# Kernel tuning notes

Hardware: AMD Instinct MI355X
Metric: run time of the kernel (lower is better)

## Reference

```python
import jax, jax.numpy as jnp
import numpy as np

N = 100000          # num nodes
E = 1250000         # num directed edges
F_IN = 64           # num_features
H = 64              # hidden_channels
C = 2               # num_classes


def gcn_layer(x, W, b, src, dst, num_nodes):
    """PyG-style GCNConv: add self-loops, symmetric norm, scatter-add aggregation."""
    loop = jnp.arange(num_nodes)
    src2 = jnp.concatenate([src, loop])   # [E+N]
    dst2 = jnp.concatenate([dst, loop])
    deg = jax.ops.segment_sum(jnp.ones_like(dst2, dtype=x.dtype), dst2,
                              num_segments=num_nodes)          # in-degree incl self-loop
    dinv = jax.lax.rsqrt(jnp.maximum(deg, 1.0))                # deg >= 1 due to self-loops
    norm = dinv[src2] * dinv[dst2]                             # [E+N]
    h = x @ W                                                  # [N, out]
    out = jax.ops.segment_sum(norm[:, None] * h[src2], dst2,
                              num_segments=num_nodes)          # [N, out]
    return out + b


def setup_inputs() -> dict:
    key = jax.random.key(0)
    ks = jax.random.split(key, 8)
    x = jax.random.normal(ks[0], (N, F_IN), dtype=jnp.float32)
    edge_index = jax.random.randint(ks[1], (2, E), 0, N, dtype=jnp.int64)
    batch = jnp.zeros((N,), dtype=jnp.int64)
    s1 = 1.0 / np.sqrt(F_IN)
    s2 = 1.0 / np.sqrt(H)
    W1 = jax.random.uniform(ks[2], (F_IN, H), jnp.float32, -s1, s1)
    b1 = jnp.zeros((H,), jnp.float32)
    W2 = jax.random.uniform(ks[3], (H, H), jnp.float32, -s2, s2)
    b2 = jnp.zeros((H,), jnp.float32)
    Wlin = jax.random.uniform(ks[4], (H, C), jnp.float32, -s2, s2)
    blin = jax.random.uniform(ks[5], (C,), jnp.float32, -s2, s2)
    return {"x": x, "edge_index": edge_index, "batch": batch,
            "W1": W1, "b1": b1, "W2": W2, "b2": b2,
            "Wlin": Wlin, "blin": blin}


def reference(x, edge_index, batch, W1, b1, W2, b2, Wlin, blin):
    src, dst = edge_index[0], edge_index[1]
    h = gcn_layer(x, W1, b1, src, dst, N)
    h = jax.nn.relu(h)
    h = gcn_layer(h, W2, b2, src, dst, N)
    # dropout p=0.5 is identity in eval mode
    return h @ Wlin + blin  # [N, C]
```

## Files before the change

kernel.cpp:

```cpp
#include <hip/hip_runtime.h>
#include <hip/hip_bf16.h>


#define FDIM 64
#define BKT_BITS 8
#define BKT 256
#define CAP 4096
#define CHUNK 2048

typedef short s16x8 __attribute__((ext_vector_type(8)));
typedef float f32x4 __attribute__((ext_vector_type(4)));

__device__ __forceinline__ unsigned short f2b(float f) {
    unsigned u = __float_as_uint(f);
    u += 0x7fff + ((u >> 16) & 1);
    return (unsigned short)(u >> 16);
}
__device__ __forceinline__ void unpk(unsigned u, float& lo, float& hi) {
    lo = __uint_as_float(u << 16);
    hi = __uint_as_float(u & 0xffff0000u);
}
__device__ __forceinline__ unsigned packb(float lo, float hi) {
    return (unsigned)f2b(lo) | ((unsigned)f2b(hi) << 16);
}
__device__ __forceinline__ unsigned relu2(unsigned u) {
    unsigned t = (u >> 15) & 0x00010001u;
    return u & ~(t * 0xFFFFu);
}

__global__ __launch_bounds__(256) void k_zero_g(int* __restrict__ g, int nb) {
    int i = blockIdx.x * blockDim.x + threadIdx.x;
    if (i < nb) g[i] = 0;
}

__global__ __launch_bounds__(256) void k_part(const int* __restrict__ src,
                                              const int* __restrict__ dst,
                                              int* __restrict__ gcnt,
                                              unsigned* __restrict__ rec,
                                              int nE, int nb) {
    __shared__ int lh[512];
    __shared__ int rc[512];
    int t = threadIdx.x;
    for (int b = t; b < nb; b += 256) lh[b] = 0;
    __syncthreads();
    int e0 = blockIdx.x * CHUNK;
    int e1 = min(nE, e0 + CHUNK);
    int myb[8];
    unsigned myr[8];
#pragma unroll
    for (int j = 0; j < 8; ++j) {
        int i = e0 + t + j * 256;
        if (i < e1) {
            int d = dst[i];
            int s = src[i];
            int b = d >> BKT_BITS;
            myb[j] = b;
            myr[j] = (unsigned)s | ((unsigned)(d & (BKT - 1)) << 17);
            atomicAdd(&lh[b], 1);
        } else {
            myb[j] = -1;
        }
    }
    __syncthreads();
    for (int b = t; b < nb; b += 256) {
        int c = lh[b];
        rc[b] = b * CAP + (c ? atomicAdd(&gcnt[b], c) : 0);
    }
    __syncthreads();
#pragma unroll
    for (int j = 0; j < 8; ++j) {
        int b = myb[j];
        if (b >= 0) {
            int pos = atomicAdd(&rc[b], 1);
            if (pos < (b + 1) * CAP)
                rec[pos] = myr[j];
        }
    }
}

__global__ __launch_bounds__(256) void k_bfill(const unsigned* __restrict__ rec,
                                               const int* __restrict__ gcnt,
                                               int* __restrict__ rowptr,
                                               float* __restrict__ dinv,
                                               int* __restrict__ col,
                                               int n, int nb, int nE) {
    __shared__ int deg[BKT];
    __shared__ int cur[BKT];
    __shared__ int wt[4];
    __shared__ int sbase;
    int b = blockIdx.x, t = threadIdx.x;
    if (t < 64) {
        int s = 0;
        for (int i = t; i < b; i += 64) s += gcnt[i];
#pragma unroll
        for (int off = 32; off >= 1; off >>= 1) s += __shfl_xor(s, off);
        if (t == 0) sbase = s;
    }
    deg[t] = 0;
    if (b == nb - 1 && t == 0) rowptr[n] = nE;
    __syncthreads();
    int rb = b * CAP;
    int re = rb + min(gcnt[b], CAP);
    for (int i = rb + t; i < re; i += 256)
        atomicAdd(&deg[rec[i] >> 17], 1);
    __syncthreads();
    {
        int d0 = deg[t];
        int lane = t & 63, w = t >> 6;
        int inc = d0;
#pragma unroll
        for (int off = 1; off < 64; off <<= 1) {
            int x = __shfl_up(inc, off);
            if (lane >= off) inc += x;
        }
        if (lane == 63) wt[w] = inc;
        __syncthreads();
        int woff = 0;
        for (int i = 0; i < w; ++i) woff += wt[i];
        int ex = sbase + woff + (inc - d0);
        int node = b * BKT + t;
        if (node < n) { rowptr[node] = ex; dinv[node] = rsqrtf((float)(d0 + 1)); }
        cur[t] = ex;
    }
    __syncthreads();
    for (int i = rb + t; i < re; i += 256) {
        unsigned u = rec[i];
        int pos = atomicAdd(&cur[u >> 17], 1);
        col[pos] = (int)(u & 0x1FFFF);
    }
}

template <int INBF>
__global__ __launch_bounds__(256) void k_gemm_mfma(const void* __restrict__ Xv,
                                                   const float* __restrict__ W,
                                                   const float* __restrict__ dinv,
                                                   unsigned short* __restrict__ Yb,
                                                   int n) {
    int t = threadIdx.x, lane = t & 63;
    int ln = lane & 15;
    int kq = lane >> 4;
    int wave = (blockIdx.x * blockDim.x + t) >> 6;
    int nw = (gridDim.x * blockDim.x) >> 6;

    s16x8 bf[4][2];
#pragma unroll
    for (int nc = 0; nc < 4; ++nc) {
#pragma unroll
        for (int kc = 0; kc < 2; ++kc) {
            s16x8 s;
#pragma unroll
            for (int i = 0; i < 8; ++i) {
                int k = kc * 32 + kq * 8 + i;
                s[i] = (short)f2b(W[k * FDIM + nc * 16 + ln]);
            }
            bf[nc][kc] = s;
        }
    }

    int ntile = (n + 15) >> 4;
    for (int tile = wave; tile < ntile; tile += nw) {
        int rowbase = tile << 4;
        int arow = rowbase + ln;
        if (arow >= n) arow = n - 1;
        s16x8 a0, a1;
        if (INBF) {
            const unsigned short* Xb = (const unsigned short*)Xv;
            uint4 u0 = *(const uint4*)&Xb[(size_t)arow * FDIM + kq * 8];
            uint4 u1 = *(const uint4*)&Xb[(size_t)arow * FDIM + 32 + kq * 8];
            u0.x = relu2(u0.x); u0.y = relu2(u0.y); u0.z = relu2(u0.z); u0.w = relu2(u0.w);
            u1.x = relu2(u1.x); u1.y = relu2(u1.y); u1.z = relu2(u1.z); u1.w = relu2(u1.w);
            a0 = *reinterpret_cast<const s16x8*>(&u0);
            a1 = *reinterpret_cast<const s16x8*>(&u1);
        } else {
            const float* Xf = (const float*)Xv;
            const float* p = Xf + (size_t)arow * FDIM + kq * 8;
            float4 f0 = *(const float4*)p;
            float4 f1 = *(const float4*)(p + 4);
            float4 f2 = *(const float4*)(p + 32);
            float4 f3 = *(const float4*)(p + 36);
            a0[0] = (short)f2b(f0.x); a0[1] = (short)f2b(f0.y);
            a0[2] = (short)f2b(f0.z); a0[3] = (short)f2b(f0.w);
            a0[4] = (short)f2b(f1.x); a0[5] = (short)f2b(f1.y);
            a0[6] = (short)f2b(f1.z); a0[7] = (short)f2b(f1.w);
            a1[0] = (short)f2b(f2.x); a1[1] = (short)f2b(f2.y);
            a1[2] = (short)f2b(f2.z); a1[3] = (short)f2b(f2.w);
            a1[4] = (short)f2b(f3.x); a1[5] = (short)f2b(f3.y);
            a1[6] = (short)f2b(f3.z); a1[7] = (short)f2b(f3.w);
        }
        f32x4 acc[4];
#pragma unroll
        for (int nc = 0; nc < 4; ++nc) {
            f32x4 z = {0.f, 0.f, 0.f, 0.f};
            acc[nc] = __builtin_amdgcn_mfma_f32_16x16x32_bf16(a0, bf[nc][0], z, 0, 0, 0);
            acc[nc] = __builtin_amdgcn_mfma_f32_16x16x32_bf16(a1, bf[nc][1], acc[nc], 0, 0, 0);
        }
        int r0 = rowbase + kq * 4;
        float dd[4];
#pragma unroll
        for (int j = 0; j < 4; ++j) {
            int r = r0 + j;
            dd[j] = dinv[r < n ? r : (n - 1)];
        }
#pragma unroll
        for (int nc = 0; nc < 4; ++nc) {
#pragma unroll
            for (int j = 0; j < 4; ++j) {
                int r = r0 + j;
                if (r < n)
                    Yb[(size_t)r * FDIM + nc * 16 + ln] = f2b(acc[nc][j] * dd[j]);
            }
        }
    }
}

template <int HEAD>
__global__ __launch_bounds__(256) void k_gather(const unsigned short* __restrict__ Hsb,
                                                const float* __restrict__ dinv,
                                                const int* __restrict__ rowptr,
                                                const int* __restrict__ col,
                                                const float* __restrict__ bias,
                                                const float* __restrict__ Wlin,
                                                const float* __restrict__ blin,
                                                void* __restrict__ outp, int n) {
    int t = threadIdx.x, lane = t & 63;
    int g = lane >> 3;
    int fl = (lane & 7) * 8;
    int wave = (blockIdx.x * blockDim.x + t) >> 6;
    int nw = (gridDim.x * blockDim.x) >> 6;
    float4 blA = *(const float4*)&bias[fl];
    float4 blB = *(const float4*)&bias[fl + 4];
    float4 q0, q1, q2, q3;
    float bl0 = 0.f, bl1 = 0.f;
    if (HEAD) {
        q0 = *(const float4*)&Wlin[fl * 2];
        q1 = *(const float4*)&Wlin[fl * 2 + 4];
        q2 = *(const float4*)&Wlin[fl * 2 + 8];
        q3 = *(const float4*)&Wlin[fl * 2 + 12];
        bl0 = blin[0]; bl1 = blin[1];
    }
    for (int r0 = wave * 8; r0 < n; r0 += nw * 8) {
        int row = r0 + g;
        bool ok = row < n;
        int rr = ok ? row : (n - 1);
        int beg = rowptr[rr], end = rowptr[rr + 1];
        uint4 sv = *(const uint4*)&Hsb[(size_t)rr * FDIM + fl];
        float a0, a1, a2, a3, a4, a5, a6, a7;
        unpk(sv.x, a0, a1); unpk(sv.y, a2, a3);
        unpk(sv.z, a4, a5); unpk(sv.w, a6, a7);
        int c0[8];
#pragma unroll
        for (int j = 0; j < 8; ++j) c0[j] = 0;
        if (beg < end) {
#pragma unroll
            for (int j = 0; j < 8; ++j) {
                int kk = beg + j;
                c0[j] = col[kk < end ? kk : beg];
            }
        }
        for (int k = beg; k < end; k += 8) {
            int kn = k + 8;
            int c1[8];
#pragma unroll
            for (int j = 0; j < 8; ++j) {
                int kk = kn + j;
                c1[j] = (kn < end) ? col[kk < end ? kk : kn] : 0;
            }
            uint4 h[8];
#pragma unroll
            for (int j = 0; j < 8; ++j)
                h[j] = *(const uint4*)&Hsb[(size_t)c0[j] * FDIM + fl];
#pragma unroll
            for (int j = 0; j < 8; ++j) {
                if (k + j < end) {
                    float l0, l1, l2, l3, l4, l5, l6, l7;
                    unpk(h[j].x, l0, l1); unpk(h[j].y, l2, l3);
                    unpk(h[j].z, l4, l5); unpk(h[j].w, l6, l7);
                    a0 += l0; a1 += l1; a2 += l2; a3 += l3;
                    a4 += l4; a5 += l5; a6 += l6; a7 += l7;
                }
            }
#pragma unroll
            for (int j = 0; j < 8; ++j) c0[j] = c1[j];
        }
        float dd = dinv[rr];
        float v0 = fmaf(dd, a0, blA.x), v1 = fmaf(dd, a1, blA.y);
        float v2 = fmaf(dd, a2, blA.z), v3 = fmaf(dd, a3, blA.w);
        float v4 = fmaf(dd, a4, blB.x), v5 = fmaf(dd, a5, blB.y);
        float v6 = fmaf(dd, a6, blB.z), v7 = fmaf(dd, a7, blB.w);
        if (HEAD == 0) {
            if (ok) {
                unsigned short* ob = (unsigned short*)outp;
                uint4 o;
                o.x = packb(v0, v1); o.y = packb(v2, v3);
                o.z = packb(v4, v5); o.w = packb(v6, v7);
                *(uint4*)&ob[(size_t)row * FDIM + fl] = o;
            }
        } else {
            float p0 = v0 * q0.x + v1 * q0.z + v2 * q1.x + v3 * q1.z
                     + v4 * q2.x + v5 * q2.z + v6 * q3.x + v7 * q3.z;
            float p1 = v0 * q0.y + v1 * q0.w + v2 * q1.y + v3 * q1.w
                     + v4 * q2.y + v5 * q2.w + v6 * q3.y + v7 * q3.w;
#pragma unroll
            for (int m = 4; m >= 1; m >>= 1) {
                p0 += __shfl_xor(p0, m);
                p1 += __shfl_xor(p1, m);
            }
            if (ok && (lane & 7) == 0) {
                float* of = (float*)outp;
                of[(size_t)row * 2 + 0] = p0 + bl0;
                of[(size_t)row * 2 + 1] = p1 + bl1;
            }
        }
    }
}

extern "C" void kernel_launch(void* const* d_in, const int* in_sizes, int n_in,
                              void* d_out, int out_size, void* d_ws, size_t ws_size,
                              hipStream_t stream) {
    const float* x    = (const float*)d_in[0];
    const int*   ei   = (const int*)d_in[1];
    const float* W1   = (const float*)d_in[3];
    const float* b1   = (const float*)d_in[4];
    const float* W2   = (const float*)d_in[5];
    const float* b2   = (const float*)d_in[6];
    const float* Wlin = (const float*)d_in[7];
    const float* blin = (const float*)d_in[8];
    float* out = (float*)d_out;

    const int n  = in_sizes[0] / FDIM;
    const int nE = in_sizes[1] / 2;
    const int* src = ei;
    const int* dst = ei + nE;
    const int NBUK = (n + BKT - 1) / BKT;

    int nPad = ((n + 1024) / 1024) * 1024;
    int nEPad = ((nE + 1023) / 1024) * 1024;
    int*      gcnt   = (int*)d_ws;
    unsigned* rec    = (unsigned*)(gcnt + 1024);
    int*      rowptr = (int*)(rec + (size_t)NBUK * CAP);
    float*    dinv   = (float*)(rowptr + nPad);
    int*      col    = (int*)(dinv + nPad);
    unsigned short* Hsb  = (unsigned short*)(col + nEPad);
    unsigned short* midb = Hsb + (size_t)nPad * FDIM;

    const int TB = 256;
    int blkP = (nE + CHUNK - 1) / CHUNK;

    k_zero_g<<<(NBUK + TB - 1) / TB, TB, 0, stream>>>(gcnt, NBUK);
    k_part<<<blkP, TB, 0, stream>>>(src, dst, gcnt, rec, nE, NBUK);
    k_bfill<<<NBUK, TB, 0, stream>>>(rec, gcnt, rowptr, dinv, col, n, NBUK, nE);

    k_gemm_mfma<0><<<512, TB, 0, stream>>>(x, W1, dinv, Hsb, n);
    k_gather<0><<<2048, TB, 0, stream>>>(Hsb, dinv, rowptr, col, b1, nullptr, nullptr, midb, n);

    k_gemm_mfma<1><<<512, TB, 0, stream>>>(midb, W2, dinv, Hsb, n);
    k_gather<1><<<2048, TB, 0, stream>>>(Hsb, dinv, rowptr, col, b2, Wlin, blin, out, n);

    (void)ws_size; (void)n_in; (void)out_size;
}
```

Before: 132.2 us.

## Fuse CSR build into one cooperative kernel with grid syncs

```diff
diff --git a/kernel.cpp b/kernel.cpp
--- a/kernel.cpp
+++ b/kernel.cpp
@@ -1,5 +1,8 @@
 #include <hip/hip_runtime.h>
 #include <hip/hip_bf16.h>
+#include <hip/hip_cooperative_groups.h>
+
+namespace cg = cooperative_groups;
 
 
 #define FDIM 64
@@ -28,105 +31,119 @@
     return u & ~(t * 0xFFFFu);
 }
 
-__global__ __launch_bounds__(256) void k_zero_g(int* __restrict__ g, int nb) {
-    int i = blockIdx.x * blockDim.x + threadIdx.x;
-    if (i < nb) g[i] = 0;
-}
-
-__global__ __launch_bounds__(256) void k_part(const int* __restrict__ src,
-                                              const int* __restrict__ dst,
-                                              int* __restrict__ gcnt,
-                                              unsigned* __restrict__ rec,
-                                              int nE, int nb) {
+__global__ __launch_bounds__(256) void k_csr(const int* __restrict__ src,
+                                             const int* __restrict__ dst,
+                                             int* __restrict__ gcnt,
+                                             unsigned* __restrict__ rec,
+                                             int* __restrict__ rowptr,
+                                             float* __restrict__ dinv,
+                                             int* __restrict__ col,
+                                             int n, int nE, int nb) {
     __shared__ int lh[512];
     __shared__ int rc[512];
+    __shared__ int wt4[4];
+    __shared__ int sbase;
+    cg::grid_group grid = cg::this_grid();
     int t = threadIdx.x;
-    for (int b = t; b < nb; b += 256) lh[b] = 0;
+    int b = blockIdx.x;
+
+    int gi = b * 256 + t;
+    if (gi < nb) gcnt[gi] = 0;
+    grid.sync();
+
+    for (int i = t; i < nb; i += 256) lh[i] = 0;
     __syncthreads();
-    int e0 = blockIdx.x * CHUNK;
-    int e1 = min(nE, e0 + CHUNK);
+    int e0 = b * CHUNK;
+    int i0 = e0 + t * 8;
     int myb[8];
     unsigned myr[8];
+    if (i0 + 8 <= nE) {
+        int4 s0 = *(const int4*)&src[i0];
+        int4 s1 = *(const int4*)&src[i0 + 4];
+        int4 d0 = *(const int4*)&dst[i0];
+        int4 d1 = *(const int4*)&dst[i0 + 4];
+        int ss[8] = {s0.x, s0.y, s0.z, s0.w, s1.x, s1.y, s1.z, s1.w};
+        int dd[8] = {d0.x, d0.y, d0.z, d0.w, d1.x, d1.y, d1.z, d1.w};
+#pragma unroll
+        for (int j = 0; j < 8; ++j) {
+            int d = dd[j];
+            myb[j] = d >> BKT_BITS;
+            myr[j] = (unsigned)ss[j] | ((unsigned)(d & (BKT - 1)) << 17);
+            atomicAdd(&lh[myb[j]], 1);
+        }
+    } else {
+#pragma unroll
+        for (int j = 0; j < 8; ++j) {
+            int i = i0 + j;
+            if (i < nE) {
+                int d = dst[i];
+                myb[j] = d >> BKT_BITS;
+                myr[j] = (unsigned)src[i] | ((unsigned)(d & (BKT - 1)) << 17);
+                atomicAdd(&lh[myb[j]], 1);
+            } else {
+                myb[j] = -1;
+            }
+        }
+    }
+    __syncthreads();
+    for (int i = t; i < nb; i += 256) {
+        int c = lh[i];
+        rc[i] = i * CAP + (c ? atomicAdd(&gcnt[i], c) : 0);
+    }
+    __syncthreads();
 #pragma unroll
     for (int j = 0; j < 8; ++j) {
-        int i = e0 + t + j * 256;
-        if (i < e1) {
-            int d = dst[i];
-            int s = src[i];
-            int b = d >> BKT_BITS;
-            myb[j] = b;
-            myr[j] = (unsigned)s | ((unsigned)(d & (BKT - 1)) << 17);
-            atomicAdd(&lh[b], 1);
-        } else {
-            myb[j] = -1;
-        }
-    }
-    __syncthreads();
-    for (int b = t; b < nb; b += 256) {
-        int c = lh[b];
-        rc[b] = b * CAP + (c ? atomicAdd(&gcnt[b], c) : 0);
-    }
-    __syncthreads();
-#pragma unroll
-    for (int j = 0; j < 8; ++j) {
-        int b = myb[j];
-        if (b >= 0) {
-            int pos = atomicAdd(&rc[b], 1);
-            if (pos < (b + 1) * CAP)
+        int bk = myb[j];
+        if (bk >= 0) {
+            int pos = atomicAdd(&rc[bk], 1);
+            if (pos < (bk + 1) * CAP)
                 rec[pos] = myr[j];
         }
     }
-}
-
-__global__ __launch_bounds__(256) void k_bfill(const unsigned* __restrict__ rec,
-                                               const int* __restrict__ gcnt,
-                                               int* __restrict__ rowptr,
-                                               float* __restrict__ dinv,
-                                               int* __restrict__ col,
-                                               int n, int nb, int nE) {
-    __shared__ int deg[BKT];
-    __shared__ int cur[BKT];
-    __shared__ int wt[4];
-    __shared__ int sbase;
-    int b = blockIdx.x, t = threadIdx.x;
-    if (t < 64) {
-        int s = 0;
-        for (int i = t; i < b; i += 64) s += gcnt[i];
-#pragma unroll
-        for (int off = 32; off >= 1; off >>= 1) s += __shfl_xor(s, off);
-        if (t == 0) sbase = s;
-    }
-    deg[t] = 0;
-    if (b == nb - 1 && t == 0) rowptr[n] = nE;
-    __syncthreads();
-    int rb = b * CAP;
-    int re = rb + min(gcnt[b], CAP);
-    for (int i = rb + t; i < re; i += 256)
-        atomicAdd(&deg[rec[i] >> 17], 1);
-    __syncthreads();
-    {
-        int d0 = deg[t];
-        int lane = t & 63, w = t >> 6;
-        int inc = d0;
-#pragma unroll
-        for (int off = 1; off < 64; off <<= 1) {
-            int x = __shfl_up(inc, off);
-            if (lane >= off) inc += x;
-        }
-        if (lane == 63) wt[w] = inc;
+    grid.sync();
+
+    if (b < nb) {
+        int* deg = lh;
+        int* cur = rc;
+        if (t < 64) {
+            int s = 0;
+            for (int i = t; i < b; i += 64) s += gcnt[i];
+#pragma unroll
+            for (int off = 32; off >= 1; off >>= 1) s += __shfl_xor(s, off);
+            if (t == 0) sbase = s;
+        }
+        deg[t] = 0;
+        if (b == nb - 1 && t == 0) rowptr[n] = nE;
         __syncthreads();
-        int woff = 0;
-        for (int i = 0; i < w; ++i) woff += wt[i];
-        int ex = sbase + woff + (inc - d0);
-        int node = b * BKT + t;
-        if (node < n) { rowptr[node] = ex; dinv[node] = rsqrtf((float)(d0 + 1)); }
-        cur[t] = ex;
-    }
-    __syncthreads();
-    for (int i = rb + t; i < re; i += 256) {
-        unsigned u = rec[i];
-        int pos = atomicAdd(&cur[u >> 17], 1);
-        col[pos] = (int)(u & 0x1FFFF);
+        int rb = b * CAP;
+        int re = rb + min(gcnt[b], CAP);
+        for (int i = rb + t; i < re; i += 256)
+            atomicAdd(&deg[rec[i] >> 17], 1);
+        __syncthreads();
+        {
+            int d0 = deg[t];
+            int lane = t & 63, w = t >> 6;
+            int inc = d0;
+#pragma unroll
+            for (int off = 1; off < 64; off <<= 1) {
+                int x = __shfl_up(inc, off);
+                if (lane >= off) inc += x;
+            }
+            if (lane == 63) wt4[w] = inc;
+            __syncthreads();
+            int woff = 0;
+            for (int i = 0; i < w; ++i) woff += wt4[i];
+            int ex = sbase + woff + (inc - d0);
+            int node = b * BKT + t;
+            if (node < n) { rowptr[node] = ex; dinv[node] = rsqrtf((float)(d0 + 1)); }
+            cur[t] = ex;
+        }
+        __syncthreads();
+        for (int i = rb + t; i < re; i += 256) {
+            unsigned u = rec[i];
+            int pos = atomicAdd(&cur[u >> 17], 1);
+            col[pos] = (int)(u & 0x1FFFF);
+        }
     }
 }
 
@@ -247,28 +264,14 @@
         float a0, a1, a2, a3, a4, a5, a6, a7;
         unpk(sv.x, a0, a1); unpk(sv.y, a2, a3);
         unpk(sv.z, a4, a5); unpk(sv.w, a6, a7);
-        int c0[8];
-#pragma unroll
-        for (int j = 0; j < 8; ++j) c0[j] = 0;
-        if (beg < end) {
+        for (int k = beg; k < end; k += 8) {
+            uint4 h[8];
 #pragma unroll
             for (int j = 0; j < 8; ++j) {
-                int kk = beg + j;
-                c0[j] = col[kk < end ? kk : beg];
-            }
-        }
-        for (int k = beg; k < end; k += 8) {
-            int kn = k + 8;
-            int c1[8];
-#pragma unroll
-            for (int j = 0; j < 8; ++j) {
-                int kk = kn + j;
-                c1[j] = (kn < end) ? col[kk < end ? kk : kn] : 0;
-            }
-            uint4 h[8];
-#pragma unroll
-            for (int j = 0; j < 8; ++j)
-                h[j] = *(const uint4*)&Hsb[(size_t)c0[j] * FDIM + fl];
+                int kk = k + j;
+                int s = col[kk < end ? kk : beg];
+                h[j] = *(const uint4*)&Hsb[(size_t)s * FDIM + fl];
+            }
 #pragma unroll
             for (int j = 0; j < 8; ++j) {
                 if (k + j < end) {
@@ -279,8 +282,6 @@
                     a4 += l4; a5 += l5; a6 += l6; a7 += l7;
                 }
             }
-#pragma unroll
-            for (int j = 0; j < 8; ++j) c0[j] = c1[j];
         }
         float dd = dinv[rr];
         float v0 = fmaf(dd, a0, blA.x), v1 = fmaf(dd, a1, blA.y);
@@ -346,9 +347,13 @@
     const int TB = 256;
     int blkP = (nE + CHUNK - 1) / CHUNK;
 
-    k_zero_g<<<(NBUK + TB - 1) / TB, TB, 0, stream>>>(gcnt, NBUK);
-    k_part<<<blkP, TB, 0, stream>>>(src, dst, gcnt, rec, nE, NBUK);
-    k_bfill<<<NBUK, TB, 0, stream>>>(rec, gcnt, rowptr, dinv, col, n, NBUK, nE);
+    {
+        int nn = n, ne = nE, nb = NBUK;
+        void* args[] = {(void*)&src, (void*)&dst, (void*)&gcnt, (void*)&rec,
+                        (void*)&rowptr, (void*)&dinv, (void*)&col,
+                        (void*)&nn, (void*)&ne, (void*)&nb};
+        hipLaunchCooperativeKernel((void*)k_csr, dim3(blkP), dim3(TB), args, 0, stream);
+    }
 
     k_gemm_mfma<0><<<512, TB, 0, stream>>>(x, W1, dinv, Hsb, n);
     k_gather<0><<<2048, TB, 0, stream>>>(Hsb, dinv, rowptr, col, b1, nullptr, nullptr, midb, n);
```

Result: slower. 260.3 us (+96.8%).
